# Optimization experiments

Measured on AMD Instinct MI355X. Metric: run time of the kernel, lower is better.

## Reference

```python
import jax, jax.numpy as jnp
import numpy as np

N = 50000
E = 800000
IN_C, HID, HEADS, CLS = 128, 64, 5, 40
NEG_SLOPE = 0.2


def gat_conv(h, src, dst, W, a_src, a_dst, bias, heads, out_c, concat):
    n = h.shape[0]
    hp = (h @ W).reshape(n, heads, out_c)            # [N,H,C]
    a_s = jnp.sum(hp * a_src, axis=-1)               # [N,H]
    a_d = jnp.sum(hp * a_dst, axis=-1)               # [N,H]
    e = jax.nn.leaky_relu(a_s[src] + a_d[dst], NEG_SLOPE)  # [Etot,H]
    m = jax.ops.segment_max(e, dst, num_segments=n)  # segment softmax over dst
    e = jnp.exp(e - m[dst])
    s = jax.ops.segment_sum(e, dst, num_segments=n)
    alpha = e / (s[dst] + 1e-16)                     # [Etot,H]
    msg = hp[src] * alpha[:, :, None]                # [Etot,H,C]
    out = jax.ops.segment_sum(msg, dst, num_segments=n)
    if concat:
        out = out.reshape(n, heads * out_c)
    else:
        out = out.mean(axis=1)
    return out + bias


def setup_inputs() -> dict:
    key = jax.random.key(0)
    ks = jax.random.split(key, 12)
    x = jax.random.normal(ks[0], (N, IN_C), dtype=jnp.float32)
    edge_index = jax.random.randint(ks[1], (2, E), 0, N, dtype=jnp.int64)
    g = 0.1
    return {
        "x": x,
        "edge_index": edge_index,
        "emb_W": jax.random.normal(ks[2], (IN_C, HID), jnp.float32) * g,
        "emb_b": jnp.zeros((HID,), jnp.float32),
        "W1": jax.random.normal(ks[3], (HID, HEADS * HID), jnp.float32) * g,
        "att_src1": jax.random.normal(ks[4], (HEADS, HID), jnp.float32) * g,
        "att_dst1": jax.random.normal(ks[5], (HEADS, HID), jnp.float32) * g,
        "b1": jnp.zeros((HEADS * HID,), jnp.float32),
        "W2": jax.random.normal(ks[6], (HEADS * HID, HEADS * CLS), jnp.float32) * g,
        "att_src2": jax.random.normal(ks[7], (HEADS, CLS), jnp.float32) * g,
        "att_dst2": jax.random.normal(ks[8], (HEADS, CLS), jnp.float32) * g,
        "b2": jnp.zeros((CLS,), jnp.float32),
    }


def reference(x, edge_index, emb_W, emb_b, W1, att_src1, att_dst1, b1,
              W2, att_src2, att_dst2, b2):
    n = x.shape[0]
    loops = jnp.arange(n, dtype=edge_index.dtype)
    src = jnp.concatenate([edge_index[0], loops])  # PyG adds self-loops
    dst = jnp.concatenate([edge_index[1], loops])
    h = x @ emb_W + emb_b
    emb = h
    # dropout skipped (eval mode)
    h = jax.nn.elu(gat_conv(h, src, dst, W1, att_src1, att_dst1, b1, HEADS, HID, True))
    h = gat_conv(h, src, dst, W2, att_src2, att_dst2, b2, HEADS, CLS, False)
    return emb, jax.nn.log_softmax(h, axis=1)
```

## Files before the change

### kernel.cpp

```cpp
#include <hip/hip_runtime.h>
#include <math.h>

constexpr int N_NODES = 50000;
constexpr int E_EDGES = 800000;
constexpr int ETOT    = E_EDGES + N_NODES;
constexpr int IN_C    = 128;
constexpr int HID     = 64;
constexpr int HEADS   = 5;
constexpr int CLS     = 40;
constexpr int SLOTW   = 96;
constexpr float NEG_SLOPE = 0.2f;

typedef __attribute__((ext_vector_type(8))) short short8;
typedef __attribute__((ext_vector_type(4))) float float4v;

__device__ __forceinline__ float lrelu(float v) {
    return v > 0.f ? v : NEG_SLOPE * v;
}
__device__ __forceinline__ float bf2f(unsigned short u) {
    return __uint_as_float(((unsigned)u) << 16);
}
__device__ __forceinline__ unsigned short f2bf(float f) {
    unsigned u = __float_as_uint(f);
    return (unsigned short)((u + 0x7fffu + ((u >> 16) & 1u)) >> 16);
}

__device__ __forceinline__ void pack_one(const float* __restrict__ B,
                                         unsigned short* __restrict__ Bp,
                                         int N, int KS, int t)
{
    int lane = t & 63;
    int f = (t >> 6) & 3;
    int rest = t >> 8;
    int ks = rest % KS;
    int nt = rest / KS;
    int n = nt * 64 + f * 16 + (lane & 15);
    int kbase = ks * 32 + (lane >> 4) * 8;
    unsigned short vals[8];
    #pragma unroll
    for (int j = 0; j < 8; j++) {
        float v = (n < N) ? B[(long)(kbase + j) * N + n] : 0.f;
        vals[j] = f2bf(v);
    }
    *(ushort4*)(Bp + (long)t * 8)     = make_ushort4(vals[0], vals[1], vals[2], vals[3]);
    *(ushort4*)(Bp + (long)t * 8 + 4) = make_ushort4(vals[4], vals[5], vals[6], vals[7]);
}

__global__ void build_graph(const int* __restrict__ ei, int* __restrict__ cnt,
                            unsigned short* __restrict__ slots,
                            const float* __restrict__ W0, const float* __restrict__ W1,
                            const float* __restrict__ W2,
                            const float* __restrict__ att1s, const float* __restrict__ att1d,
                            const float* __restrict__ att2s, const float* __restrict__ att2d,
                            unsigned short* __restrict__ Bp0,
                            unsigned short* __restrict__ Bp1,
                            unsigned short* __restrict__ Bp2,
                            float* __restrict__ u1s, float* __restrict__ u1d,
                            float* __restrict__ u2s, float* __restrict__ u2d)
{
    int t = blockIdx.x * blockDim.x + threadIdx.x;
    if (t < 13824) {
        if (t < 1024)      pack_one(W0, Bp0, 64,  4,  t);
        else if (t < 3584) pack_one(W1, Bp1, 320, 2,  t - 1024);
        else               pack_one(W2, Bp2, 200, 10, t - 3584);
    } else if (t < 14464) {
        int i = t - 13824;
        bool isd = i >= 320;
        int j = isd ? i - 320 : i;
        int h = j >> 6, k = j & 63;
        const float* att = isd ? att1d : att1s;
        float sum = 0.f;
        for (int c = 0; c < 64; c++)
            sum += W1[k * 320 + h * 64 + c] * att[h * 64 + c];
        (isd ? u1d : u1s)[j] = sum;
    } else if (t < 17664) {
        int i = t - 14464;
        bool isd = i >= 1600;
        int j = isd ? i - 1600 : i;
        int h = j / 320, k = j % 320;
        const float* att = isd ? att2d : att2s;
        float sum = 0.f;
        for (int c = 0; c < 40; c++)
            sum += W2[k * 200 + h * 40 + c] * att[h * 40 + c];
        (isd ? u2d : u2s)[j] = sum;
    }
    if (t >= ETOT) return;
    int s, d;
    if (t < E_EDGES) { s = ei[t]; d = ei[E_EDGES + t]; }
    else             { s = d = t - E_EDGES; }
    int pos = atomicAdd(&cnt[d], 1);
    if (pos < SLOTW) slots[d * SLOTW + pos] = (unsigned short)s;
}

__global__ __launch_bounds__(256) void gemm_mfma_emb(
    const float* __restrict__ A, const unsigned short* __restrict__ Bp,
    const float* __restrict__ bias,
    const float* __restrict__ u1s, const float* __restrict__ u1d,
    float* __restrict__ Cf, unsigned short* __restrict__ Cb,
    float* __restrict__ a_s1, float* __restrict__ a_d1, int M)
{
    const int K = 128, KS = 4;
    const int w = threadIdx.x >> 6, lane = threadIdx.x & 63;
    const int cl = lane & 15, kq = lane >> 4;
    int rowA = blockIdx.x * 64 + w * 16 + cl;
    if (rowA >= M) rowA = M - 1;
    const float* ap = A + (long)rowA * K + kq * 8;
    const unsigned short* bp = Bp + lane * 8;
    float4v acc[4] = {};
    #pragma unroll
    for (int ks = 0; ks < KS; ks++) {
        float4 u0 = *(const float4*)(ap + ks * 32);
        float4 u1 = *(const float4*)(ap + ks * 32 + 4);
        short8 a;
        a[0] = f2bf(u0.x); a[1] = f2bf(u0.y); a[2] = f2bf(u0.z); a[3] = f2bf(u0.w);
        a[4] = f2bf(u1.x); a[5] = f2bf(u1.y); a[6] = f2bf(u1.z); a[7] = f2bf(u1.w);
        #pragma unroll
        for (int f = 0; f < 4; f++) {
            short8 b = *(const short8*)(bp + ks * 2048 + f * 512);
            acc[f] = __builtin_amdgcn_mfma_f32_16x16x32_bf16(a, b, acc[f], 0, 0, 0);
        }
    }
    int rbase = blockIdx.x * 64 + w * 16 + kq * 4;
    float bc4[4];
    #pragma unroll
    for (int f = 0; f < 4; f++) {
        int col = f * 16 + cl;
        float bc = bias[col];
        bc4[f] = bc;
        #pragma unroll
        for (int r = 0; r < 4; r++) {
            int row = rbase + r;
            if (row < M) {
                float v = acc[f][r] + bc;
                Cf[(long)row * 64 + col] = v;
                Cb[(long)row * 64 + col] = f2bf(v);
            }
        }
    }
    #pragma unroll
    for (int h = 0; h < HEADS; h++) {
        float us[4], ud[4];
        #pragma unroll
        for (int f = 0; f < 4; f++) {
            us[f] = u1s[h * 64 + f * 16 + cl];
            ud[f] = u1d[h * 64 + f * 16 + cl];
        }
        #pragma unroll
        for (int r = 0; r < 4; r++) {
            float ps = 0.f, pd = 0.f;
            #pragma unroll
            for (int f = 0; f < 4; f++) {
                float v = acc[f][r] + bc4[f];
                ps += v * us[f];
                pd += v * ud[f];
            }
            #pragma unroll
            for (int off = 1; off < 16; off <<= 1) {
                ps += __shfl_xor(ps, off);
                pd += __shfl_xor(pd, off);
            }
            int row = rbase + r;
            if (cl == 0 && row < M) {
                a_s1[row * 5 + h] = ps;
                a_d1[row * 5 + h] = pd;
            }
        }
    }
}

__global__ __launch_bounds__(256) void aggr1_new(
    const int* __restrict__ cnt, const unsigned short* __restrict__ slots,
    const float* __restrict__ a_s, const float* __restrict__ a_d,
    const unsigned short* __restrict__ emb, unsigned short* __restrict__ e_out)
{
    __shared__ float alph[4][64 * 8];
    int wid = (blockIdx.x * blockDim.x + threadIdx.x) >> 6;
    int w = threadIdx.x >> 6;
    int lane = threadIdx.x & 63;
    if (wid >= N_NODES) return;
    int deg = cnt[wid];
    if (deg > SLOTW) deg = SLOTW;
    const unsigned short* myslot = slots + wid * SLOTW;

    float adh[HEADS];
    #pragma unroll
    for (int h = 0; h < HEADS; h++) adh[h] = a_d[wid * HEADS + h];

    const char* embB = (const char*)emb;
    float acc[HEADS] = {};

    if (deg <= 64) {
        bool has = lane < deg;
        int s = has ? (int)myslot[lane] : 0;
        int rowoff = s * 128;
        float v[HEADS], mx[HEADS], sm[HEADS];
        #pragma unroll
        for (int h = 0; h < HEADS; h++) {
            v[h] = has ? lrelu(a_s[s * HEADS + h] + adh[h]) : -1e30f;
            mx[h] = v[h];
        }
        #pragma unroll
        for (int h = 0; h < HEADS; h++)
            #pragma unroll
            for (int off = 32; off; off >>= 1)
                mx[h] = fmaxf(mx[h], __shfl_xor(mx[h], off));
        #pragma unroll
        for (int h = 0; h < HEADS; h++) {
            float e = has ? __expf(v[h] - mx[h]) : 0.f;
            v[h] = e;
            sm[h] = e;
        }
        #pragma unroll
        for (int h = 0; h < HEADS; h++)
            #pragma unroll
            for (int off = 32; off; off >>= 1)
                sm[h] += __shfl_xor(sm[h], off);
        if (has) {
            #pragma unroll
            for (int h = 0; h < HEADS; h++)
                alph[w][lane * 8 + h] = v[h] / (sm[h] + 1e-16f);
        }
        int i = 0;
        for (; i + 7 < deg; i += 8) {
            float fv[8]; float4 a4[8]; float a1[8];
            #pragma unroll
            for (int k = 0; k < 8; k++) {
                int off = __shfl(rowoff, i + k);
                unsigned short q = *(const unsigned short*)(embB + off + lane * 2);
                fv[k] = bf2f(q);
                a4[k] = *(const float4*)&alph[w][(i + k) * 8];
                a1[k] = alph[w][(i + k) * 8 + 4];
            }
            #pragma unroll
            for (int k = 0; k < 8; k++) {
                acc[0] += fv[k] * a4[k].x;
                acc[1] += fv[k] * a4[k].y;
                acc[2] += fv[k] * a4[k].z;
                acc[3] += fv[k] * a4[k].w;
                acc[4] += fv[k] * a1[k];
            }
        }
        for (; i < deg; i++) {
            int off = __shfl(rowoff, i);
            float fv = bf2f(*(const unsigned short*)(embB + off + lane * 2));
            float4 a4 = *(const float4*)&alph[w][i * 8];
            float a1 = alph[w][i * 8 + 4];
            acc[0] += fv * a4.x;
            acc[1] += fv * a4.y;
            acc[2] += fv * a4.z;
            acc[3] += fv * a4.w;
            acc[4] += fv * a1;
        }
    } else {
        float mx[HEADS], inv[HEADS], sm[HEADS] = {};
        #pragma unroll
        for (int h = 0; h < HEADS; h++) mx[h] = -1e30f;
        for (int e = lane; e < deg; e += 64) {
            int s = myslot[e];
            #pragma unroll
            for (int h = 0; h < HEADS; h++)
                mx[h] = fmaxf(mx[h], lrelu(a_s[s * HEADS + h] + adh[h]));
        }
        #pragma unroll
        for (int h = 0; h < HEADS; h++)
            #pragma unroll
            for (int off = 32; off; off >>= 1)
                mx[h] = fmaxf(mx[h], __shfl_xor(mx[h], off));
        for (int e = lane; e < deg; e += 64) {
            int s = myslot[e];
            #pragma unroll
            for (int h = 0; h < HEADS; h++)
                sm[h] += __expf(lrelu(a_s[s * HEADS + h] + adh[h]) - mx[h]);
        }
        #pragma unroll
        for (int h = 0; h < HEADS; h++) {
            #pragma unroll
            for (int off = 32; off; off >>= 1)
                sm[h] += __shfl_xor(sm[h], off);
            inv[h] = 1.f / (sm[h] + 1e-16f);
        }
        for (int e = 0; e < deg; e++) {
            int s0 = myslot[e];
            float fv = bf2f(*(const unsigned short*)(embB + s0 * 128 + lane * 2));
            #pragma unroll
            for (int h = 0; h < HEADS; h++) {
                float a0 = __expf(lrelu(a_s[s0 * HEADS + h] + adh[h]) - mx[h]) * inv[h];
                acc[h] += fv * a0;
            }
        }
    }

    #pragma unroll
    for (int h = 0; h < HEADS; h++)
        e_out[(long)wid * 320 + h * 64 + lane] = f2bf(acc[h]);
}

__global__ __launch_bounds__(256) void gemm_mix1(
    const unsigned short* __restrict__ A, const unsigned short* __restrict__ Bp,
    const float* __restrict__ bias,
    const float* __restrict__ u2s, const float* __restrict__ u2d,
    unsigned short* __restrict__ C, float* __restrict__ a_s2,
    float* __restrict__ a_d2, int M)
{
    const int w = threadIdx.x >> 6, lane = threadIdx.x & 63;
    const int cl = lane & 15, kq = lane >> 4;
    int rowA = blockIdx.x * 64 + w * 16 + cl;
    if (rowA >= M) rowA = M - 1;
    const unsigned short* ap = A + (long)rowA * 320;
    const unsigned short* bp = Bp + lane * 8;
    float4v acc[20] = {};
    #pragma unroll
    for (int nt = 0; nt < 5; nt++)
        #pragma unroll
        for (int ks = 0; ks < 2; ks++) {
            short8 a = *(const short8*)(ap + nt * 64 + ks * 32 + kq * 8);
            #pragma unroll
            for (int f = 0; f < 4; f++) {
                short8 b = *(const short8*)(bp + (nt * 2 + ks) * 2048 + f * 512);
                acc[nt * 4 + f] =
                    __builtin_amdgcn_mfma_f32_16x16x32_bf16(a, b, acc[nt * 4 + f], 0, 0, 0);
            }
        }
    int rbase = blockIdx.x * 64 + w * 16 + kq * 4;
    #pragma unroll
    for (int nt = 0; nt < 5; nt++)
        #pragma unroll
        for (int f = 0; f < 4; f++) {
            int col = nt * 64 + f * 16 + cl;
            float bc = bias[col];
            #pragma unroll
            for (int r = 0; r < 4; r++) {
                float v = acc[nt * 4 + f][r] + bc;
                v = v > 0.f ? v : __expf(v) - 1.f;
                acc[nt * 4 + f][r] = v;
                int row = rbase + r;
                if (row < M) C[(long)row * 320 + col] = f2bf(v);
            }
        }
    #pragma unroll
    for (int h = 0; h < HEADS; h++) {
        float us[20], ud[20];
        #pragma unroll
        for (int nt = 0; nt < 5; nt++)
            #pragma unroll
            for (int f = 0; f < 4; f++) {
                us[nt * 4 + f] = u2s[h * 320 + nt * 64 + f * 16 + cl];
                ud[nt * 4 + f] = u2d[h * 320 + nt * 64 + f * 16 + cl];
            }
        #pragma unroll
        for (int r = 0; r < 4; r++) {
            float ps = 0.f, pd = 0.f;
            #pragma unroll
            for (int j = 0; j < 20; j++) {
                ps += acc[j][r] * us[j];
                pd += acc[j][r] * ud[j];
            }
            #pragma unroll
            for (int off = 1; off < 16; off <<= 1) {
                ps += __shfl_xor(ps, off);
                pd += __shfl_xor(pd, off);
            }
            int row = rbase + r;
            if (cl == 0 && row < M) {
                a_s2[row * 5 + h] = ps;
                a_d2[row * 5 + h] = pd;
            }
        }
    }
}

__global__ __launch_bounds__(256) void gemm_mfma_l2(
    const unsigned short* __restrict__ A, const unsigned short* __restrict__ Bp,
    unsigned short* __restrict__ C, int M)
{
    const int K = 320, KS = 10;
    const int w = threadIdx.x >> 6, lane = threadIdx.x & 63;
    const int cl = lane & 15, kq = lane >> 4;
    int rowA = blockIdx.x * 64 + w * 16 + cl;
    if (rowA >= M) rowA = M - 1;
    const unsigned short* ap = A + (long)rowA * K + kq * 8;
    const unsigned short* bp = Bp + lane * 8;
    float4v acc[16] = {};
    for (int ks = 0; ks < KS; ks++) {
        short8 a = *(const short8*)(ap + ks * 32);
        #pragma unroll
        for (int nt = 0; nt < 4; nt++)
            #pragma unroll
            for (int f = 0; f < 4; f++) {
                short8 b = *(const short8*)(bp + (nt * KS + ks) * 2048 + f * 512);
                acc[nt * 4 + f] =
                    __builtin_amdgcn_mfma_f32_16x16x32_bf16(a, b, acc[nt * 4 + f], 0, 0, 0);
            }
    }
    int rbase = blockIdx.x * 64 + w * 16 + kq * 4;
    #pragma unroll
    for (int nt = 0; nt < 4; nt++)
        #pragma unroll
        for (int f = 0; f < 4; f++) {
            int col = nt * 64 + f * 16 + cl;
            if (col >= 200) continue;
            #pragma unroll
            for (int r = 0; r < 4; r++) {
                int row = rbase + r;
                if (row < M) C[(long)row * 200 + col] = f2bf(acc[nt * 4 + f][r]);
            }
        }
}

__global__ __launch_bounds__(256) void aggr2_fused(
    const int* __restrict__ cnt, const unsigned short* __restrict__ slots,
    const float* __restrict__ a_s, const float* __restrict__ a_d,
    const unsigned short* __restrict__ hp, const float* __restrict__ bias,
    float* __restrict__ out)
{
    __shared__ float alph[4][320];
    int wid = (blockIdx.x * blockDim.x + threadIdx.x) >> 6;
    int w = threadIdx.x >> 6;
    int lane = threadIdx.x & 63;
    if (wid >= N_NODES) return;
    int deg = cnt[wid];
    if (deg > SLOTW) deg = SLOTW;
    const unsigned short* myslot = slots + wid * SLOTW;

    float adh[HEADS];
    #pragma unroll
    for (int h = 0; h < HEADS; h++) adh[h] = a_d[wid * HEADS + h];

    const bool act = lane < 50;
    const int ch4 = lane * 4;
    const int hq  = act ? lane / 10 : 0;
    const char* hpB = (const char*)hp;
    float acc0 = 0.f, acc1 = 0.f, acc2 = 0.f, acc3 = 0.f;

    if (deg <= 64) {
        bool has = lane < deg;
        int s = has ? (int)myslot[lane] : 0;
        int rowoff = s * 400;
        float v[HEADS], mx[HEADS], sm[HEADS];
        #pragma unroll
        for (int h = 0; h < HEADS; h++) {
            v[h] = has ? lrelu(a_s[s * HEADS + h] + adh[h]) : -1e30f;
            mx[h] = v[h];
        }
        #pragma unroll
        for (int h = 0; h < HEADS; h++)
            #pragma unroll
            for (int off = 32; off; off >>= 1)
                mx[h] = fmaxf(mx[h], __shfl_xor(mx[h], off));
        #pragma unroll
        for (int h = 0; h < HEADS; h++) {
            float e = has ? __expf(v[h] - mx[h]) : 0.f;
            v[h] = e;
            sm[h] = e;
        }
        #pragma unroll
        for (int h = 0; h < HEADS; h++)
            #pragma unroll
            for (int off = 32; off; off >>= 1)
                sm[h] += __shfl_xor(sm[h], off);
        if (has) {
            #pragma unroll
            for (int h = 0; h < HEADS; h++)
                alph[w][lane * 5 + h] = 0.2f * v[h] / (sm[h] + 1e-16f);
        }
        int i = 0;
        for (; i + 7 < deg; i += 8) {
            ushort4 q[8]; float a[8];
            #pragma unroll
            for (int k = 0; k < 8; k++) {
                int off = __shfl(rowoff, i + k);
                q[k] = act ? *(const ushort4*)(hpB + off + ch4 * 2)
                           : make_ushort4(0, 0, 0, 0);
                a[k] = alph[w][(i + k) * 5 + hq];
            }
            #pragma unroll
            for (int k = 0; k < 8; k++) {
                acc0 += bf2f(q[k].x) * a[k];
                acc1 += bf2f(q[k].y) * a[k];
                acc2 += bf2f(q[k].z) * a[k];
                acc3 += bf2f(q[k].w) * a[k];
            }
        }
        for (; i < deg; i++) {
            int off = __shfl(rowoff, i);
            if (act) {
                ushort4 q0 = *(const ushort4*)(hpB + off + ch4 * 2);
                float a0 = alph[w][i * 5 + hq];
                acc0 += bf2f(q0.x) * a0;
                acc1 += bf2f(q0.y) * a0;
                acc2 += bf2f(q0.z) * a0;
                acc3 += bf2f(q0.w) * a0;
            }
        }
    } else {
        float mx[HEADS], inv[HEADS], sm[HEADS] = {};
        #pragma unroll
        for (int h = 0; h < HEADS; h++) mx[h] = -1e30f;
        for (int e = lane; e < deg; e += 64) {
            int s = myslot[e];
            #pragma unroll
            for (int h = 0; h < HEADS; h++)
                mx[h] = fmaxf(mx[h], lrelu(a_s[s * HEADS + h] + adh[h]));
        }
        #pragma unroll
        for (int h = 0; h < HEADS; h++)
            #pragma unroll
            for (int off = 32; off; off >>= 1)
                mx[h] = fmaxf(mx[h], __shfl_xor(mx[h], off));
        for (int e = lane; e < deg; e += 64) {
            int s = myslot[e];
            #pragma unroll
            for (int h = 0; h < HEADS; h++)
                sm[h] += __expf(lrelu(a_s[s * HEADS + h] + adh[h]) - mx[h]);
        }
        #pragma unroll
        for (int h = 0; h < HEADS; h++) {
            #pragma unroll
            for (int off = 32; off; off >>= 1)
                sm[h] += __shfl_xor(sm[h], off);
            inv[h] = 0.2f / (sm[h] + 1e-16f);
        }
        for (int e = 0; e < deg; e++) {
            int s0 = myslot[e];
            if (act) {
                ushort4 q0 = *(const ushort4*)(hpB + s0 * 400 + ch4 * 2);
                float a0 = __expf(lrelu(a_s[s0 * HEADS + hq] + adh[hq]) - mx[hq]) * inv[hq];
                acc0 += bf2f(q0.x) * a0;
                acc1 += bf2f(q0.y) * a0;
                acc2 += bf2f(q0.z) * a0;
                acc3 += bf2f(q0.w) * a0;
            }
        }
    }

    float r0 = acc0, r1 = acc1, r2 = acc2, r3 = acc3;
    #pragma unroll
    for (int h5 = 1; h5 < 5; h5++) {
        int sl = (lane + 10 * h5) & 63;
        r0 += __shfl(acc0, sl);
        r1 += __shfl(acc1, sl);
        r2 += __shfl(acc2, sl);
        r3 += __shfl(acc3, sl);
    }

    float vb0 = -1e30f, vb1 = -1e30f, vb2 = -1e30f, vb3 = -1e30f;
    if (lane < 10) {
        vb0 = r0 + bias[ch4 + 0];
        vb1 = r1 + bias[ch4 + 1];
        vb2 = r2 + bias[ch4 + 2];
        vb3 = r3 + bias[ch4 + 3];
    }
    float mxv = fmaxf(fmaxf(vb0, vb1), fmaxf(vb2, vb3));
    #pragma unroll
    for (int off = 32; off; off >>= 1)
        mxv = fmaxf(mxv, __shfl_xor(mxv, off));
    float sme = 0.f;
    if (lane < 10)
        sme = __expf(vb0 - mxv) + __expf(vb1 - mxv) +
              __expf(vb2 - mxv) + __expf(vb3 - mxv);
    #pragma unroll
    for (int off = 32; off; off >>= 1)
        sme += __shfl_xor(sme, off);
    float ls = mxv + __logf(sme);
    if (lane < 10) {
        float4 o = make_float4(vb0 - ls, vb1 - ls, vb2 - ls, vb3 - ls);
        *(float4*)(out + (long)wid * CLS + ch4) = o;
    }
}

extern "C" void kernel_launch(void* const* d_in, const int* in_sizes, int n_in,
                              void* d_out, int out_size, void* d_ws, size_t ws_size,
                              hipStream_t stream)
{
    const float* x     = (const float*)d_in[0];
    const int*   ei    = (const int*)d_in[1];
    const float* emb_W = (const float*)d_in[2];
    const float* emb_b = (const float*)d_in[3];
    const float* W1    = (const float*)d_in[4];
    const float* as1   = (const float*)d_in[5];
    const float* ad1   = (const float*)d_in[6];
    const float* b1    = (const float*)d_in[7];
    const float* W2    = (const float*)d_in[8];
    const float* as2   = (const float*)d_in[9];
    const float* ad2   = (const float*)d_in[10];
    const float* b2    = (const float*)d_in[11];

    float* out_emb = (float*)d_out;
    float* out_cls = (float*)d_out + (size_t)N_NODES * HID;

    char* ws = (char*)d_ws;
    unsigned short* e_agg  = (unsigned short*)(ws);
    unsigned short* hp2b   = (unsigned short*)(ws);
    unsigned short* h1b    = (unsigned short*)(ws + 32000000);
    unsigned short* embb   = (unsigned short*)(ws + 64000000);
    float*          a_s1   = (float*)(ws + 70400000);
    float*          a_d1   = (float*)(ws + 71400000);
    float*          a_s2   = (float*)(ws + 72400000);
    float*          a_d2   = (float*)(ws + 73400000);
    unsigned short* Bp0    = (unsigned short*)(ws + 74400000);
    unsigned short* Bp1    = (unsigned short*)(ws + 74500000);
    unsigned short* Bp2    = (unsigned short*)(ws + 74600000);
    float*          u1s    = (float*)(ws + 74800000);
    float*          u1d    = (float*)(ws + 74810000);
    float*          u2s    = (float*)(ws + 74820000);
    float*          u2d    = (float*)(ws + 74830000);
    int*            cnt    = (int*)(ws + 74840000);
    unsigned short* slots  = (unsigned short*)(ws + 75100000);

    const dim3 blk(256);
    const int eb  = (ETOT + 255) / 256;
    const int nb4 = (N_NODES + 3) / 4;
    const int mgrid = (N_NODES + 63) / 64;

    hipMemsetAsync(cnt, 0, (size_t)N_NODES * 4, stream);
    build_graph<<<eb, blk, 0, stream>>>(ei, cnt, slots, emb_W, W1, W2,
                                        as1, ad1, as2, ad2,
                                        Bp0, Bp1, Bp2, u1s, u1d, u2s, u2d);

    gemm_mfma_emb<<<mgrid, blk, 0, stream>>>(x, Bp0, emb_b, u1s, u1d,
                                             out_emb, embb, a_s1, a_d1, N_NODES);

    aggr1_new<<<nb4, blk, 0, stream>>>(cnt, slots, a_s1, a_d1, embb, e_agg);
    gemm_mix1<<<mgrid, blk, 0, stream>>>(e_agg, Bp1, b1, u2s, u2d,
                                         h1b, a_s2, a_d2, N_NODES);

    gemm_mfma_l2<<<mgrid, blk, 0, stream>>>(h1b, Bp2, hp2b, N_NODES);
    aggr2_fused<<<nb4, blk, 0, stream>>>(cnt, slots, a_s2, a_d2, hp2b, b2, out_cls);
}
```

Measured before the change: 369.7 us.

## Fuse layer-1 mix GEMM with layer-2 projection GEMM via LDS tile

Merges gemm_mix1 and gemm_mfma_l2 into one kernel. The ELU-activated hidden tile is staged in padded LDS instead of being written to global memory, then reused directly as the A operand of the second GEMM. This removes a 32MB bf16 intermediate write and read-back, plus one kernel launch. In exchange it uses about 42KB of LDS per block, which may limit occupancy. It also relies on each wave reading only the rows it wrote, with no explicit barrier.

```diff
diff --git a/kernel.cpp b/kernel.cpp
--- a/kernel.cpp
+++ b/kernel.cpp
@@ -295,19 +295,22 @@
         e_out[(long)wid * 320 + h * 64 + lane] = f2bf(acc[h]);
 }
 
-__global__ __launch_bounds__(256) void gemm_mix1(
-    const unsigned short* __restrict__ A, const unsigned short* __restrict__ Bp,
-    const float* __restrict__ bias,
+__global__ __launch_bounds__(256) void gemm_mix_l2(
+    const unsigned short* __restrict__ A, const unsigned short* __restrict__ Bp1,
+    const unsigned short* __restrict__ Bp2, const float* __restrict__ bias,
     const float* __restrict__ u2s, const float* __restrict__ u2d,
-    unsigned short* __restrict__ C, float* __restrict__ a_s2,
+    unsigned short* __restrict__ hp2, float* __restrict__ a_s2,
     float* __restrict__ a_d2, int M)
 {
+    constexpr int LDP = 328;
+    __shared__ unsigned short tile[64 * LDP];
     const int w = threadIdx.x >> 6, lane = threadIdx.x & 63;
     const int cl = lane & 15, kq = lane >> 4;
     int rowA = blockIdx.x * 64 + w * 16 + cl;
     if (rowA >= M) rowA = M - 1;
     const unsigned short* ap = A + (long)rowA * 320;
-    const unsigned short* bp = Bp + lane * 8;
+    const unsigned short* bp1 = Bp1 + lane * 8;
+
     float4v acc[20] = {};
     #pragma unroll
     for (int nt = 0; nt < 5; nt++)
@@ -316,12 +319,13 @@
             short8 a = *(const short8*)(ap + nt * 64 + ks * 32 + kq * 8);
             #pragma unroll
             for (int f = 0; f < 4; f++) {
-                short8 b = *(const short8*)(bp + (nt * 2 + ks) * 2048 + f * 512);
+                short8 b = *(const short8*)(bp1 + (nt * 2 + ks) * 2048 + f * 512);
                 acc[nt * 4 + f] =
                     __builtin_amdgcn_mfma_f32_16x16x32_bf16(a, b, acc[nt * 4 + f], 0, 0, 0);
             }
         }
     int rbase = blockIdx.x * 64 + w * 16 + kq * 4;
+    const int lrow = w * 16 + kq * 4;
     #pragma unroll
     for (int nt = 0; nt < 5; nt++)
         #pragma unroll
@@ -333,8 +337,7 @@
                 float v = acc[nt * 4 + f][r] + bc;
                 v = v > 0.f ? v : __expf(v) - 1.f;
                 acc[nt * 4 + f][r] = v;
-                int row = rbase + r;
-                if (row < M) C[(long)row * 320 + col] = f2bf(v);
+                tile[(lrow + r) * LDP + col] = f2bf(v);
             }
         }
     #pragma unroll
@@ -367,32 +370,22 @@
             }
         }
     }
-}
-
-__global__ __launch_bounds__(256) void gemm_mfma_l2(
-    const unsigned short* __restrict__ A, const unsigned short* __restrict__ Bp,
-    unsigned short* __restrict__ C, int M)
-{
-    const int K = 320, KS = 10;
-    const int w = threadIdx.x >> 6, lane = threadIdx.x & 63;
-    const int cl = lane & 15, kq = lane >> 4;
-    int rowA = blockIdx.x * 64 + w * 16 + cl;
-    if (rowA >= M) rowA = M - 1;
-    const unsigned short* ap = A + (long)rowA * K + kq * 8;
-    const unsigned short* bp = Bp + lane * 8;
-    float4v acc[16] = {};
-    for (int ks = 0; ks < KS; ks++) {
-        short8 a = *(const short8*)(ap + ks * 32);
+
+    const unsigned short* bp2 = Bp2 + lane * 8;
+    const unsigned short* arow = tile + (w * 16 + cl) * LDP;
+    float4v acc2[16] = {};
+    #pragma unroll
+    for (int ks = 0; ks < 10; ks++) {
+        short8 a2 = *(const short8*)(arow + ks * 32 + kq * 8);
         #pragma unroll
         for (int nt = 0; nt < 4; nt++)
             #pragma unroll
             for (int f = 0; f < 4; f++) {
-                short8 b = *(const short8*)(bp + (nt * KS + ks) * 2048 + f * 512);
-                acc[nt * 4 + f] =
-                    __builtin_amdgcn_mfma_f32_16x16x32_bf16(a, b, acc[nt * 4 + f], 0, 0, 0);
-            }
-    }
-    int rbase = blockIdx.x * 64 + w * 16 + kq * 4;
+                short8 b = *(const short8*)(bp2 + (nt * 10 + ks) * 2048 + f * 512);
+                acc2[nt * 4 + f] =
+                    __builtin_amdgcn_mfma_f32_16x16x32_bf16(a2, b, acc2[nt * 4 + f], 0, 0, 0);
+            }
+    }
     #pragma unroll
     for (int nt = 0; nt < 4; nt++)
         #pragma unroll
@@ -402,7 +395,7 @@
             #pragma unroll
             for (int r = 0; r < 4; r++) {
                 int row = rbase + r;
-                if (row < M) C[(long)row * 200 + col] = f2bf(acc[nt * 4 + f][r]);
+                if (row < M) hp2[(long)row * 200 + col] = f2bf(acc2[nt * 4 + f][r]);
             }
         }
 }
@@ -590,8 +583,7 @@
 
     char* ws = (char*)d_ws;
     unsigned short* e_agg  = (unsigned short*)(ws);
-    unsigned short* hp2b   = (unsigned short*)(ws);
-    unsigned short* h1b    = (unsigned short*)(ws + 32000000);
+    unsigned short* hp2b   = (unsigned short*)(ws + 32000000);
     unsigned short* embb   = (unsigned short*)(ws + 64000000);
     float*          a_s1   = (float*)(ws + 70400000);
     float*          a_d1   = (float*)(ws + 71400000);
@@ -621,9 +613,9 @@
                                              out_emb, embb, a_s1, a_d1, N_NODES);
 
     aggr1_new<<<nb4, blk, 0, stream>>>(cnt, slots, a_s1, a_d1, embb, e_agg);
-    gemm_mix1<<<mgrid, blk, 0, stream>>>(e_agg, Bp1, b1, u2s, u2d,
-                                         h1b, a_s2, a_d2, N_NODES);
-
-    gemm_mfma_l2<<<mgrid, blk, 0, stream>>>(h1b, Bp2, hp2b, N_NODES);
+
+    gemm_mix_l2<<<mgrid, blk, 0, stream>>>(e_agg, Bp1, Bp2, b1, u2s, u2d,
+                                           hp2b, a_s2, a_d2, N_NODES);
+
     aggr2_fused<<<nb4, blk, 0, stream>>>(cnt, slots, a_s2, a_d2, hp2b, b2, out_cls);
 }
```

Measured after the change: 368.5 us. No clear change (-0.3%).
